# Optimization experiments

Measured on AMD Instinct MI355X. Metric: run time of the kernel, lower is better.

## Reference

```python
import jax, jax.numpy as jnp
import numpy as np

B, S = 512, 64          # batch, grain grid size (coarse==medium==fine==64, see notes)
N = S * S               # tokens per image
CONTENT_PAD, CONTENT_EOS = 1024, 1025
COARSE_POS_PAD, COARSE_POS_EOS = 128, 129
MEDIUM_POS_PAD, MEDIUM_POS_EOS = 256, 257
FINE_POS_PAD, FINE_POS_EOS = 1024, 1025


def setup_inputs() -> dict:
    key = jax.random.key(0)
    k1, k2 = jax.random.split(key)
    indices = jax.random.randint(k1, (B, S, S), 0, 1024, dtype=jnp.int32)
    grain_indices = jax.random.randint(k2, (B, S, S), 0, 3, dtype=jnp.int32)
    return {"indices": indices, "grain_indices": grain_indices}


def _compact(vals, mask, eos, pad):
    """Stable stream-compaction per row: selected vals first, then EOS, then PAD.
    vals/mask: [B, N].  Output: [B, N+1] (static max length; torch pads to batch max)."""
    b, n = vals.shape
    # stable argsort of (not mask) brings True positions to the front, in order
    order = jnp.argsort(jnp.where(mask, 0, 1).astype(jnp.int32), axis=1, stable=True)
    sel = jnp.take_along_axis(vals, order, axis=1)                  # [B, N]
    sel = jnp.concatenate([sel, jnp.zeros((b, 1), vals.dtype)], axis=1)  # [B, N+1]
    cnt = jnp.sum(mask.astype(jnp.int32), axis=1, keepdims=True)    # [B, 1]
    slot = jnp.arange(n + 1, dtype=jnp.int32)[None, :]              # [1, N+1]
    out = jnp.where(slot < cnt, sel,
                    jnp.where(slot == cnt, jnp.asarray(eos, vals.dtype),
                              jnp.asarray(pad, vals.dtype)))
    return out


def reference(indices, grain_indices):
    b, s, _ = indices.shape
    n = s * s
    # With coarse==medium==fine the module's rearranges are identity reshapes:
    # coarse_content = medium_content source = fine_content source = flattened grid,
    # and all three position sequences are row-major arange(n).
    flat = indices.reshape(b, n)
    g = grain_indices.reshape(b, n)
    pos = jnp.broadcast_to(jnp.arange(n, dtype=indices.dtype), (b, n))

    coarse_content = _compact(flat, g == 0, CONTENT_EOS, CONTENT_PAD)
    coarse_position = _compact(pos, g == 0, COARSE_POS_EOS, COARSE_POS_PAD)
    medium_content = _compact(flat, g == 1, CONTENT_EOS, CONTENT_PAD)
    medium_position = _compact(pos, g == 1, MEDIUM_POS_EOS, MEDIUM_POS_PAD)
    fine_content = _compact(flat, g == 2, CONTENT_EOS, CONTENT_PAD)
    fine_position = _compact(pos, g == 2, FINE_POS_EOS, FINE_POS_PAD)

    coarse_segment = jnp.zeros_like(coarse_content)
    medium_segment = jnp.ones_like(medium_content)
    fine_segment = jnp.full_like(fine_content, 2)
    return (coarse_content, medium_content, fine_content,
            coarse_position, medium_position, fine_position,
            coarse_segment, medium_segment, fine_segment)
```

## Files before the change

### kernel.cpp

```cpp
#include <hip/hip_runtime.h>


constexpr int N_TOK  = 4096;
constexpr int M_OUT  = N_TOK + 1;
constexpr int TPB    = 1024;
constexpr int NWAVES = TPB / 64;
constexpr int EPT    = N_TOK / TPB;

constexpr int CONTENT_PAD = 1024, CONTENT_EOS = 1025;
__device__ __constant__ int POS_PAD[3] = {128, 256, 1024};
__device__ __constant__ int POS_EOS[3] = {129, 257, 1025};

__device__ __forceinline__ int swz(int a) { return a ^ ((a >> 3) & 0x1C); }

__global__ __launch_bounds__(TPB, 8) void
triple_grain_permute(const int* __restrict__ indices,
                     const int* __restrict__ grain,
                     int* __restrict__ out,
                     int batch) {
    const int b = blockIdx.x;
    const int t = threadIdx.x;
    const int lane = t & 63;
    const int wave = t >> 6;

    const int* idx_row = indices + (size_t)b * N_TOK;
    const int* g_row   = grain   + (size_t)b * N_TOK;

    __shared__ int s_packed[N_TOK];
    __shared__ unsigned int s_wave_tot[NWAVES];

    const int4 gg = reinterpret_cast<const int4*>(g_row)[t];
    const int4 ii = reinterpret_cast<const int4*>(idx_row)[t];

    const size_t ARR = (size_t)batch * M_OUT;
    const int peel = (4 - (b & 3)) & 3;
    const int nch  = (M_OUT - peel) >> 2;
    const int rem  = (M_OUT - peel) & 3;
    const int s0   = peel + 4 * t;

#pragma unroll
    for (int c = 0; c < 3; ++c) {
        int* dst_s = out + (size_t)(6 + c) * ARR + (size_t)b * M_OUT;
        if (t < peel) dst_s[t] = c;
        if (t < nch)  *reinterpret_cast<int4*>(dst_s + s0) = make_int4(c, c, c, c);
        if (t < rem)  dst_s[M_OUT - rem + t] = c;
    }

    int gv[EPT] = {gg.x, gg.y, gg.z, gg.w};
    const int elem0 = t * EPT;
    int pv[EPT] = {ii.x | (elem0 << 12),
                   ii.y | ((elem0 + 1) << 12),
                   ii.z | ((elem0 + 2) << 12),
                   ii.w | ((elem0 + 3) << 12)};

    int c0 = 0, c1 = 0, c2 = 0;
#pragma unroll
    for (int j = 0; j < EPT; ++j) {
        c0 += (gv[j] == 0);
        c1 += (gv[j] == 1);
        c2 += (gv[j] == 2);
    }
    unsigned int packed = (unsigned)c0 | ((unsigned)c1 << 10) | ((unsigned)c2 << 20);

    unsigned int inc = packed;
#pragma unroll
    for (int off = 1; off < 64; off <<= 1) {
        unsigned int nb = (unsigned int)__shfl_up((int)inc, off, 64);
        if (lane >= off) inc += nb;
    }
    if (lane == 63) s_wave_tot[wave] = inc;

    asm volatile("s_waitcnt lgkmcnt(0)" ::: "memory");
    __builtin_amdgcn_s_barrier();
    __builtin_amdgcn_sched_barrier(0);

    int wp0 = 0, wp1 = 0, wp2 = 0, tot0 = 0, tot1 = 0, tot2 = 0;
#pragma unroll
    for (int w = 0; w < NWAVES; ++w) {
        const unsigned int v = s_wave_tot[w];
        const int f0 = v & 1023, f1 = (v >> 10) & 1023, f2 = (v >> 20) & 1023;
        if (w < wave) { wp0 += f0; wp1 += f1; wp2 += f2; }
        tot0 += f0; tot1 += f1; tot2 += f2;
    }
    const unsigned int exv = inc - packed;
    const int o0 = wp0 + (int)(exv & 1023);
    const int o1 = wp1 + (int)((exv >> 10) & 1023);
    const int o2 = wp2 + (int)((exv >> 20) & 1023);
    const int cnt0 = tot0, cnt1 = tot1, cnt2 = tot2;
    const int base0 = 0, base1 = cnt0, base2 = cnt0 + cnt1;

    const int bases[3] = {base0, base1, base2};
    const int cnts[3]  = {cnt0, cnt1, cnt2};

#pragma unroll
    for (int c = 0; c < 3; ++c) {
        if (t < nch && s0 > cnts[c]) {
            int* dst_c = out + (size_t)c       * ARR + (size_t)b * M_OUT;
            int* dst_p = out + (size_t)(3 + c) * ARR + (size_t)b * M_OUT;
            *reinterpret_cast<int4*>(dst_c + s0) =
                make_int4(CONTENT_PAD, CONTENT_PAD, CONTENT_PAD, CONTENT_PAD);
            const int pp = POS_PAD[c];
            *reinterpret_cast<int4*>(dst_p + s0) = make_int4(pp, pp, pp, pp);
        }
    }

    int d0 = base0 + o0, d1 = base1 + o1, d2 = base2 + o2;
#pragma unroll
    for (int j = 0; j < EPT; ++j) {
        const int cl = gv[j];
        const int dst = (cl == 0) ? d0 : ((cl == 1) ? d1 : d2);
        s_packed[swz(dst)] = pv[j];
        d0 += (cl == 0);
        d1 += (cl == 1);
        d2 += (cl == 2);
    }

    asm volatile("s_waitcnt lgkmcnt(0)" ::: "memory");
    __builtin_amdgcn_s_barrier();
    __builtin_amdgcn_sched_barrier(0);

#pragma unroll
    for (int c = 0; c < 3; ++c) {
        int* dst_c = out + (size_t)c       * ARR + (size_t)b * M_OUT;
        int* dst_p = out + (size_t)(3 + c) * ARR + (size_t)b * M_OUT;
        const int cnt = cnts[c];
        const int base = bases[c];
        const int peos = POS_EOS[c], ppad = POS_PAD[c];

        auto elem = [&](int slot, int& vc, int& vp) {
            int a = base + slot;
            a = (a > N_TOK - 1) ? (N_TOK - 1) : a;
            const int pk = s_packed[swz(a)];
            vc = (slot < cnt) ? (pk & 0xFFF) : ((slot == cnt) ? CONTENT_EOS : CONTENT_PAD);
            vp = (slot < cnt) ? (pk >> 12)   : ((slot == cnt) ? peos : ppad);
        };

        if (t < peel) {
            int vc, vp;
            elem(t, vc, vp);
            dst_c[t] = vc; dst_p[t] = vp;
        }
        if (t < nch) {
            if (s0 + 3 < cnt) {
                const int a = base + s0;
                const int p0 = s_packed[swz(a)];
                const int p1 = s_packed[swz(a + 1)];
                const int p2 = s_packed[swz(a + 2)];
                const int p3 = s_packed[swz(a + 3)];
                *reinterpret_cast<int4*>(dst_c + s0) =
                    make_int4(p0 & 0xFFF, p1 & 0xFFF, p2 & 0xFFF, p3 & 0xFFF);
                *reinterpret_cast<int4*>(dst_p + s0) =
                    make_int4(p0 >> 12, p1 >> 12, p2 >> 12, p3 >> 12);
            } else if (s0 <= cnt) {
                int4 vc4, vp4;
                elem(s0 + 0, vc4.x, vp4.x);
                elem(s0 + 1, vc4.y, vp4.y);
                elem(s0 + 2, vc4.z, vp4.z);
                elem(s0 + 3, vc4.w, vp4.w);
                *reinterpret_cast<int4*>(dst_c + s0) = vc4;
                *reinterpret_cast<int4*>(dst_p + s0) = vp4;
            }
        }
        if (t < rem) {
            const int slot = M_OUT - rem + t;
            int vc, vp;
            elem(slot, vc, vp);
            dst_c[slot] = vc; dst_p[slot] = vp;
        }
    }
}

extern "C" void kernel_launch(void* const* d_in, const int* in_sizes, int n_in,
                              void* d_out, int out_size, void* d_ws, size_t ws_size,
                              hipStream_t stream) {
    const int* indices = (const int*)d_in[0];
    const int* grain   = (const int*)d_in[1];
    int* out = (int*)d_out;

    const int batch = in_sizes[0] / N_TOK;
    triple_grain_permute<<<batch, TPB, 0, stream>>>(indices, grain, out, batch);
}
```

Before: 108.4 us.

## Split segment-fill writes into separate blocks and defer pad writes

Launches two blocks per batch row: one block only writes the three constant segment arrays and exits, the other does the scan/compaction. Pad writes for content/position move from before the scatter into the final write loop as a third branch, and the hand-written barrier sequences are replaced with __syncthreads. The aim is to spread the constant store traffic over more blocks and take stores off the compaction block's critical path. In exchange, twice as many blocks are launched and the per-block setup work is duplicated.

```diff
diff --git a/kernel.cpp b/kernel.cpp
--- a/kernel.cpp
+++ b/kernel.cpp
@@ -18,10 +18,28 @@
                      const int* __restrict__ grain,
                      int* __restrict__ out,
                      int batch) {
-    const int b = blockIdx.x;
+    const int b    = blockIdx.x >> 1;
+    const int role = blockIdx.x & 1;
     const int t = threadIdx.x;
     const int lane = t & 63;
     const int wave = t >> 6;
+
+    const size_t ARR = (size_t)batch * M_OUT;
+    const int peel = (4 - (b & 3)) & 3;
+    const int nch  = (M_OUT - peel) >> 2;
+    const int rem  = (M_OUT - peel) & 3;
+    const int s0   = peel + 4 * t;
+
+    if (role == 1) {
+#pragma unroll
+        for (int c = 0; c < 3; ++c) {
+            int* dst_s = out + (size_t)(6 + c) * ARR + (size_t)b * M_OUT;
+            if (t < peel) dst_s[t] = c;
+            if (t < nch)  *reinterpret_cast<int4*>(dst_s + s0) = make_int4(c, c, c, c);
+            if (t < rem)  dst_s[M_OUT - rem + t] = c;
+        }
+        return;
+    }
 
     const int* idx_row = indices + (size_t)b * N_TOK;
     const int* g_row   = grain   + (size_t)b * N_TOK;
@@ -29,23 +47,8 @@
     __shared__ int s_packed[N_TOK];
     __shared__ unsigned int s_wave_tot[NWAVES];
 
-    const int4 gg = reinterpret_cast<const int4*>(g_row)[t];
-    const int4 ii = reinterpret_cast<const int4*>(idx_row)[t];
-
-    const size_t ARR = (size_t)batch * M_OUT;
-    const int peel = (4 - (b & 3)) & 3;
-    const int nch  = (M_OUT - peel) >> 2;
-    const int rem  = (M_OUT - peel) & 3;
-    const int s0   = peel + 4 * t;
-
-#pragma unroll
-    for (int c = 0; c < 3; ++c) {
-        int* dst_s = out + (size_t)(6 + c) * ARR + (size_t)b * M_OUT;
-        if (t < peel) dst_s[t] = c;
-        if (t < nch)  *reinterpret_cast<int4*>(dst_s + s0) = make_int4(c, c, c, c);
-        if (t < rem)  dst_s[M_OUT - rem + t] = c;
-    }
-
+    int4 gg = reinterpret_cast<const int4*>(g_row)[t];
+    int4 ii = reinterpret_cast<const int4*>(idx_row)[t];
     int gv[EPT] = {gg.x, gg.y, gg.z, gg.w};
     const int elem0 = t * EPT;
     int pv[EPT] = {ii.x | (elem0 << 12),
@@ -69,10 +72,7 @@
         if (lane >= off) inc += nb;
     }
     if (lane == 63) s_wave_tot[wave] = inc;
-
-    asm volatile("s_waitcnt lgkmcnt(0)" ::: "memory");
-    __builtin_amdgcn_s_barrier();
-    __builtin_amdgcn_sched_barrier(0);
+    __syncthreads();
 
     int wp0 = 0, wp1 = 0, wp2 = 0, tot0 = 0, tot1 = 0, tot2 = 0;
 #pragma unroll
@@ -87,37 +87,23 @@
     const int o1 = wp1 + (int)((exv >> 10) & 1023);
     const int o2 = wp2 + (int)((exv >> 20) & 1023);
     const int cnt0 = tot0, cnt1 = tot1, cnt2 = tot2;
+
     const int base0 = 0, base1 = cnt0, base2 = cnt0 + cnt1;
-
-    const int bases[3] = {base0, base1, base2};
-    const int cnts[3]  = {cnt0, cnt1, cnt2};
-
-#pragma unroll
-    for (int c = 0; c < 3; ++c) {
-        if (t < nch && s0 > cnts[c]) {
-            int* dst_c = out + (size_t)c       * ARR + (size_t)b * M_OUT;
-            int* dst_p = out + (size_t)(3 + c) * ARR + (size_t)b * M_OUT;
-            *reinterpret_cast<int4*>(dst_c + s0) =
-                make_int4(CONTENT_PAD, CONTENT_PAD, CONTENT_PAD, CONTENT_PAD);
-            const int pp = POS_PAD[c];
-            *reinterpret_cast<int4*>(dst_p + s0) = make_int4(pp, pp, pp, pp);
-        }
-    }
 
     int d0 = base0 + o0, d1 = base1 + o1, d2 = base2 + o2;
 #pragma unroll
     for (int j = 0; j < EPT; ++j) {
-        const int cl = gv[j];
-        const int dst = (cl == 0) ? d0 : ((cl == 1) ? d1 : d2);
+        const int c = gv[j];
+        const int dst = (c == 0) ? d0 : ((c == 1) ? d1 : d2);
         s_packed[swz(dst)] = pv[j];
-        d0 += (cl == 0);
-        d1 += (cl == 1);
-        d2 += (cl == 2);
+        d0 += (c == 0);
+        d1 += (c == 1);
+        d2 += (c == 2);
     }
+    __syncthreads();
 
-    asm volatile("s_waitcnt lgkmcnt(0)" ::: "memory");
-    __builtin_amdgcn_s_barrier();
-    __builtin_amdgcn_sched_barrier(0);
+    const int bases[3] = {base0, base1, base2};
+    const int cnts[3]  = {cnt0, cnt1, cnt2};
 
 #pragma unroll
     for (int c = 0; c < 3; ++c) {
@@ -151,7 +137,12 @@
                     make_int4(p0 & 0xFFF, p1 & 0xFFF, p2 & 0xFFF, p3 & 0xFFF);
                 *reinterpret_cast<int4*>(dst_p + s0) =
                     make_int4(p0 >> 12, p1 >> 12, p2 >> 12, p3 >> 12);
-            } else if (s0 <= cnt) {
+            } else if (s0 > cnt) {
+                *reinterpret_cast<int4*>(dst_c + s0) =
+                    make_int4(CONTENT_PAD, CONTENT_PAD, CONTENT_PAD, CONTENT_PAD);
+                *reinterpret_cast<int4*>(dst_p + s0) =
+                    make_int4(ppad, ppad, ppad, ppad);
+            } else {
                 int4 vc4, vp4;
                 elem(s0 + 0, vc4.x, vp4.x);
                 elem(s0 + 1, vc4.y, vp4.y);
@@ -178,5 +169,5 @@
     int* out = (int*)d_out;
 
     const int batch = in_sizes[0] / N_TOK;
-    triple_grain_permute<<<batch, TPB, 0, stream>>>(indices, grain, out, batch);
+    triple_grain_permute<<<2 * batch, TPB, 0, stream>>>(indices, grain, out, batch);
 }
```

After: 97.41 us. -10.1%, faster.
